# Kernel tuning notes

Measured on AMD Instinct MI355X. Metric: run time of the kernel, lower is better.

The kernel has to match this reference:

```python
import jax, jax.numpy as jnp
import numpy as np

GROUP_SIZE = 256


def dequantize(qweight, scales, zeros, dtype):
    # qweight: [out, in] uint8-valued ints; scales/zeros: [n_groups, 1]
    out_f, in_f = qweight.shape
    w = qweight.astype(dtype).reshape(-1, GROUP_SIZE)
    w = (w - zeros) * scales
    return w.reshape(out_f, in_f)


def setup_inputs() -> dict:
    key = jax.random.key(0)
    k1, k2, k3, k4, k5 = jax.random.split(key, 5)
    B, S, IN, OUT = 4, 2048, 4096, 4096
    n_groups = OUT * IN // GROUP_SIZE
    x = jax.random.normal(k1, (B, S, IN), dtype=jnp.float32)
    qweight = jax.random.randint(k2, (OUT, IN), 0, 256, dtype=jnp.int32)
    scales = jax.random.uniform(k3, (n_groups, 1), dtype=jnp.float32) * 0.01 + 1e-4
    zeros = jax.random.randint(k4, (n_groups, 1), 0, 256).astype(jnp.float32)
    bias = jax.random.normal(k5, (OUT,), dtype=jnp.float32) * 0.02
    return {"x": x, "qweight": qweight, "scales": scales, "zeros": zeros, "bias": bias}


def reference(x, qweight, scales, zeros, bias):
    # float_weight = (qw - zeros) * scales, grouped along flattened weight
    w = dequantize(qweight, scales, zeros, x.dtype)  # [out, in]
    # y = x @ W^T + b
    return jnp.einsum("bsi,oi->bso", x, w) + bias
```

## Files before the change

### kernel.cpp

```cpp
#include <hip/hip_runtime.h>


typedef __attribute__((ext_vector_type(8))) short bf16x8;
typedef __attribute__((ext_vector_type(8))) unsigned short ushort8;
typedef __attribute__((ext_vector_type(4))) float f32x4;

__device__ inline unsigned short f2bf(float f) {
  union { float f; unsigned int u; } v; v.f = f;
  unsigned int u = v.u;
  return (unsigned short)((u + 0x7fffu + ((u >> 16) & 1u)) >> 16);
}

__global__ void prep_kernel(const int* __restrict__ q,
                            const float* __restrict__ sc,
                            const float* __restrict__ zp,
                            ushort8* __restrict__ wb,
                            const float* __restrict__ x,
                            ushort8* __restrict__ xb,
                            int nw8, int nx8) {
  int t = blockIdx.x * blockDim.x + threadIdx.x;
  if (t < nw8) {
    const int4* q4 = (const int4*)q + (size_t)t * 2;
    int4 a = q4[0];
    int4 b = q4[1];
    int g = t >> 5;
    float s = sc[g], z = zp[g];
    ushort8 o;
    o[0] = f2bf(((float)a.x - z) * s);
    o[1] = f2bf(((float)a.y - z) * s);
    o[2] = f2bf(((float)a.z - z) * s);
    o[3] = f2bf(((float)a.w - z) * s);
    o[4] = f2bf(((float)b.x - z) * s);
    o[5] = f2bf(((float)b.y - z) * s);
    o[6] = f2bf(((float)b.z - z) * s);
    o[7] = f2bf(((float)b.w - z) * s);
    wb[t] = o;
  } else {
    int u = t - nw8;
    if (u >= nx8) return;
    const float4* x4 = (const float4*)x + (size_t)u * 2;
    float4 a = x4[0];
    float4 b = x4[1];
    ushort8 o;
    o[0] = f2bf(a.x); o[1] = f2bf(a.y); o[2] = f2bf(a.z); o[3] = f2bf(a.w);
    o[4] = f2bf(b.x); o[5] = f2bf(b.y); o[6] = f2bf(b.z); o[7] = f2bf(b.w);
    xb[u] = o;
  }
}

#define BM 256
#define BN 256
#define BK 64

#define BAR() asm volatile("s_barrier" ::: "memory")
#define MFMA16(d, x, y) d = __builtin_amdgcn_mfma_f32_16x16x32_bf16(x, y, d, 0, 0, 0)

__device__ inline void gload_lds16(const void* g, void* l) {
  __builtin_amdgcn_global_load_lds(
      (const __attribute__((address_space(1))) unsigned int*)g,
      (__attribute__((address_space(3))) unsigned int*)l, 16, 0, 0);
}

__device__ inline void stage_half(const unsigned short* __restrict__ gsrc,
                                  char* lds_region, int K, int wave, int lane) {
  const int l3  = lane >> 3;
  const int swz = ((lane & 7) ^ l3) * 8;
#pragma unroll
  for (int inst = 0; inst < 2; ++inst) {
    const int row = inst * 64 + wave * 8 + l3;
    gload_lds16(gsrc + (size_t)row * K + swz,
                lds_region + (size_t)(inst * 512 + wave * 64) * 16);
  }
}

__global__ __launch_bounds__(512, 2)
void gemm256_kernel(const unsigned short* __restrict__ A,
                    const unsigned short* __restrict__ B,
                    const float* __restrict__ bias,
                    float* __restrict__ C,
                    int M, int N, int K) {
  extern __shared__ char lds[];
  const int t    = threadIdx.x;
  const int lane = t & 63;
  const int wave = t >> 6;
  const int wm   = wave >> 2;
  const int wn   = wave & 3;
  const int lr   = lane & 15;
  const int hi   = lane >> 4;
  const int l7   = lane & 7;

  const int nwg = gridDim.x;
  const int cpx = nwg >> 3;
  const int bid = blockIdx.x;
  const int swzb = (bid & 7) * cpx + (bid >> 3);
  const int ntn = N / BN;
  const int bm = swzb / ntn, bn = swzb % ntn;
  const int row0 = bm * BM, col0 = bn * BN;

  const int NT = K / BK;

  const int soff0 = ((hi) ^ l7) * 16;
  const int soff1 = ((4 + hi) ^ l7) * 16;

  const unsigned short* Asrc = A + (size_t)row0 * K;
  const unsigned short* Bsrc = B + (size_t)col0 * K;

#define STAGE_A0(buf, kt) stage_half(Asrc + (size_t)(kt) * BK,           (buf),         K, wave, lane)
#define STAGE_A1(buf, kt) stage_half(Asrc + (size_t)128 * K + (kt) * BK, (buf) + 16384, K, wave, lane)
#define STAGE_B0(buf, kt) stage_half(Bsrc + (size_t)(kt) * BK,           (buf) + 32768, K, wave, lane)
#define STAGE_B1(buf, kt) stage_half(Bsrc + (size_t)128 * K + (kt) * BK, (buf) + 49152, K, wave, lane)

  f32x4 acc[8][4] = {};
  bf16x8 a[4][2];
  bf16x8 b[4][2];

#define READ_A(mh, bufp) {                                                    \
    const char* Ab_ = (const char*)(bufp) + wm * 16384 + (mh) * 8192;         \
    _Pragma("unroll")                                                         \
    for (int mm = 0; mm < 4; ++mm) {                                          \
      const int r_ = (mm * 16 + lr) * 128;                                    \
      a[mm][0] = *(const bf16x8*)(Ab_ + r_ + soff0);                          \
      a[mm][1] = *(const bf16x8*)(Ab_ + r_ + soff1);                          \
    } }
#define READ_B(nh, bufp) {                                                    \
    const char* Bb_ = (const char*)(bufp) + 32768 + wn * 8192;                \
    _Pragma("unroll")                                                         \
    for (int nn = 0; nn < 2; ++nn) {                                          \
      const int r_ = (((nh) * 2 + nn) * 16 + lr) * 128;                       \
      b[(nh) * 2 + nn][0] = *(const bf16x8*)(Bb_ + r_ + soff0);               \
      b[(nh) * 2 + nn][1] = *(const bf16x8*)(Bb_ + r_ + soff1);               \
    } }
#define MFMA_QUAD(mh, nh)                                                     \
    __builtin_amdgcn_s_setprio(1);                                            \
    _Pragma("unroll")                                                         \
    for (int mm = 0; mm < 4; ++mm)                                            \
      _Pragma("unroll")                                                       \
      for (int nn = 0; nn < 2; ++nn) {                                        \
        MFMA16(acc[(mh) * 4 + mm][(nh) * 2 + nn], a[mm][0], b[(nh) * 2 + nn][0]); \
        MFMA16(acc[(mh) * 4 + mm][(nh) * 2 + nn], a[mm][1], b[(nh) * 2 + nn][1]); \
      }                                                                       \
    __builtin_amdgcn_s_setprio(0);

#define KT_BODY(buf, nbuf, kt, GUARDED)                                       \
  {                                                                           \
                      \
    BAR();                                                                    \
    MFMA_QUAD(0, 0);                                                          \
    if (!(GUARDED) || (kt) + 1 < NT) STAGE_A1(nbuf, (kt) + 1);                \
    READ_B(1, buf);                                                           \
                     \
    BAR();                                                                    \
    MFMA_QUAD(0, 1);                                                          \
    if (!(GUARDED) || (kt) + 2 < NT) STAGE_B0(buf, (kt) + 2);                 \
    READ_A(1, buf);                                                           \
                          \
    BAR();                                                                    \
    MFMA_QUAD(1, 0);                                                          \
    if (!(GUARDED) || (kt) + 2 < NT) {                                        \
      STAGE_B1(buf, (kt) + 2);                                                \
      asm volatile("s_waitcnt vmcnt(4)" ::: "memory");                        \
    } else {                                                                  \
      asm volatile("s_waitcnt vmcnt(0)" ::: "memory");                        \
    }                                                                         \
       \
    BAR();                                                                    \
    MFMA_QUAD(1, 1);                                                          \
    if (!(GUARDED) || (kt) + 2 < NT) STAGE_A0(buf, (kt) + 2);                 \
    if (!(GUARDED) || (kt) + 1 < NT) {                                        \
      READ_A(0, nbuf);                                                        \
      READ_B(0, nbuf);                                                        \
    }                                                                         \
  }

  char* buf0 = lds;
  char* buf1 = lds + 65536;
  STAGE_A0(buf0, 0); STAGE_A1(buf0, 0); STAGE_B0(buf0, 0); STAGE_B1(buf0, 0);
  STAGE_A0(buf1, 1); STAGE_B0(buf1, 1); STAGE_B1(buf1, 1);
  asm volatile("s_waitcnt vmcnt(6)" ::: "memory");
  BAR();
  READ_A(0, buf0);
  READ_B(0, buf0);

  int kt = 0;
  for (; kt + 3 < NT; kt += 2) {
    KT_BODY(buf0, buf1, kt, 0);
    KT_BODY(buf1, buf0, kt + 1, 0);
  }
  for (; kt < NT; ++kt) {
    char* buf  = lds + ((kt & 1) << 16);
    char* nbuf = lds + (((kt & 1) ^ 1) << 16);
    KT_BODY(buf, nbuf, kt, 1);
  }

#pragma unroll
  for (int n = 0; n < 4; ++n) {
    const int col = col0 + wn * 64 + n * 16 + lr;
    const float bv = bias[col];
#pragma unroll
    for (int m = 0; m < 8; ++m) {
      const int rbase = row0 + wm * 128 + m * 16 + hi * 4;
#pragma unroll
      for (int j = 0; j < 4; ++j)
        C[(size_t)(rbase + j) * N + col] = acc[m][n][j] + bv;
    }
  }
#undef STAGE_A0
#undef STAGE_A1
#undef STAGE_B0
#undef STAGE_B1
#undef READ_A
#undef READ_B
#undef MFMA_QUAD
#undef KT_BODY
}

extern "C" void kernel_launch(void* const* d_in, const int* in_sizes, int n_in,
                              void* d_out, int out_size, void* d_ws, size_t ws_size,
                              hipStream_t stream) {
  const float* x      = (const float*)d_in[0];
  const int*   qw     = (const int*)d_in[1];
  const float* scales = (const float*)d_in[2];
  const float* zeros  = (const float*)d_in[3];
  const float* bias   = (const float*)d_in[4];
  float* out = (float*)d_out;

  const int OUT = in_sizes[4];
  const int IN  = in_sizes[1] / OUT;
  const int M   = in_sizes[0] / IN;

  unsigned short* wb = (unsigned short*)d_ws;
  unsigned short* xb = wb + (size_t)OUT * IN;

  {
    int nw8 = OUT * IN / 8;
    int nx8 = (int)((size_t)M * IN / 8);
    int total = nw8 + nx8;
    prep_kernel<<<(total + 255) / 256, 256, 0, stream>>>(
        qw, scales, zeros, (ushort8*)wb, x, (ushort8*)xb, nw8, nx8);
  }
  {
    hipFuncSetAttribute((const void*)gemm256_kernel,
                        hipFuncAttributeMaxDynamicSharedMemorySize, 131072);
    dim3 grid((M / BM) * (OUT / BN));
    gemm256_kernel<<<grid, 512, 131072, stream>>>(xb, wb, bias, out, M, OUT, IN);
  }
}
```

Baseline: 268.7 us.

## Halve GEMM K-tile to 32 with new LDS swizzle and grid-stride prep kernel

The GEMM K tile drops from 64 to 32, which halves the double-buffered LDS footprint from 128KB to 64KB. The staging layout, swizzle pattern, fragment reads and vmcnt waits are reworked to match. The smaller footprint is meant to let two workgroups fit per CU, as the launch bounds request. The prep kernel becomes a grid-stride loop over a fixed 2048-block grid instead of one thread per 8 elements. The cost is twice as many K iterations, with more barriers and staging overhead per unit of MFMA work, and less latency hiding per stage.

```diff
diff --git a/kernel.cpp b/kernel.cpp
--- a/kernel.cpp
+++ b/kernel.cpp
@@ -18,39 +18,40 @@
                             const float* __restrict__ x,
                             ushort8* __restrict__ xb,
                             int nw8, int nx8) {
-  int t = blockIdx.x * blockDim.x + threadIdx.x;
-  if (t < nw8) {
-    const int4* q4 = (const int4*)q + (size_t)t * 2;
-    int4 a = q4[0];
-    int4 b = q4[1];
-    int g = t >> 5;
-    float s = sc[g], z = zp[g];
-    ushort8 o;
-    o[0] = f2bf(((float)a.x - z) * s);
-    o[1] = f2bf(((float)a.y - z) * s);
-    o[2] = f2bf(((float)a.z - z) * s);
-    o[3] = f2bf(((float)a.w - z) * s);
-    o[4] = f2bf(((float)b.x - z) * s);
-    o[5] = f2bf(((float)b.y - z) * s);
-    o[6] = f2bf(((float)b.z - z) * s);
-    o[7] = f2bf(((float)b.w - z) * s);
-    wb[t] = o;
-  } else {
-    int u = t - nw8;
-    if (u >= nx8) return;
-    const float4* x4 = (const float4*)x + (size_t)u * 2;
-    float4 a = x4[0];
-    float4 b = x4[1];
-    ushort8 o;
-    o[0] = f2bf(a.x); o[1] = f2bf(a.y); o[2] = f2bf(a.z); o[3] = f2bf(a.w);
-    o[4] = f2bf(b.x); o[5] = f2bf(b.y); o[6] = f2bf(b.z); o[7] = f2bf(b.w);
-    xb[u] = o;
+  const int stride = gridDim.x * blockDim.x;
+  for (int t = blockIdx.x * blockDim.x + threadIdx.x; t < nw8 + nx8; t += stride) {
+    if (t < nw8) {
+      const int4* q4 = (const int4*)q + (size_t)t * 2;
+      int4 a = q4[0];
+      int4 b = q4[1];
+      int g = t >> 5;
+      float s = sc[g], z = zp[g];
+      ushort8 o;
+      o[0] = f2bf(((float)a.x - z) * s);
+      o[1] = f2bf(((float)a.y - z) * s);
+      o[2] = f2bf(((float)a.z - z) * s);
+      o[3] = f2bf(((float)a.w - z) * s);
+      o[4] = f2bf(((float)b.x - z) * s);
+      o[5] = f2bf(((float)b.y - z) * s);
+      o[6] = f2bf(((float)b.z - z) * s);
+      o[7] = f2bf(((float)b.w - z) * s);
+      wb[t] = o;
+    } else {
+      int u = t - nw8;
+      const float4* x4 = (const float4*)x + (size_t)u * 2;
+      float4 a = x4[0];
+      float4 b = x4[1];
+      ushort8 o;
+      o[0] = f2bf(a.x); o[1] = f2bf(a.y); o[2] = f2bf(a.z); o[3] = f2bf(a.w);
+      o[4] = f2bf(b.x); o[5] = f2bf(b.y); o[6] = f2bf(b.z); o[7] = f2bf(b.w);
+      xb[u] = o;
+    }
   }
 }
 
 #define BM 256
 #define BN 256
-#define BK 64
+#define BK 32
 
 #define BAR() asm volatile("s_barrier" ::: "memory")
 #define MFMA16(d, x, y) d = __builtin_amdgcn_mfma_f32_16x16x32_bf16(x, y, d, 0, 0, 0)
@@ -61,16 +62,12 @@
       (__attribute__((address_space(3))) unsigned int*)l, 16, 0, 0);
 }
 
-__device__ inline void stage_half(const unsigned short* __restrict__ gsrc,
-                                  char* lds_region, int K, int wave, int lane) {
-  const int l3  = lane >> 3;
-  const int swz = ((lane & 7) ^ l3) * 8;
-#pragma unroll
-  for (int inst = 0; inst < 2; ++inst) {
-    const int row = inst * 64 + wave * 8 + l3;
-    gload_lds16(gsrc + (size_t)row * K + swz,
-                lds_region + (size_t)(inst * 512 + wave * 64) * 16);
-  }
+__device__ inline void stage_unit32(const unsigned short* __restrict__ gsrc,
+                                    char* lds_region, int K, int wave, int lane) {
+  const int row  = wave * 16 + (lane >> 2);
+  const int slot = (lane & 3) ^ ((row >> 1) & 3);
+  gload_lds16(gsrc + (size_t)row * K + slot * 8,
+              lds_region + (size_t)wave * 1024);
 }
 
 __global__ __launch_bounds__(512, 2)
@@ -87,7 +84,6 @@
   const int wn   = wave & 3;
   const int lr   = lane & 15;
   const int hi   = lane >> 4;
-  const int l7   = lane & 7;
 
   const int nwg = gridDim.x;
   const int cpx = nwg >> 3;
@@ -99,46 +95,39 @@
 
   const int NT = K / BK;
 
-  const int soff0 = ((hi) ^ l7) * 16;
-  const int soff1 = ((4 + hi) ^ l7) * 16;
+  const int soff = (hi ^ ((lr >> 1) & 3)) * 16;
 
   const unsigned short* Asrc = A + (size_t)row0 * K;
   const unsigned short* Bsrc = B + (size_t)col0 * K;
 
-#define STAGE_A0(buf, kt) stage_half(Asrc + (size_t)(kt) * BK,           (buf),         K, wave, lane)
-#define STAGE_A1(buf, kt) stage_half(Asrc + (size_t)128 * K + (kt) * BK, (buf) + 16384, K, wave, lane)
-#define STAGE_B0(buf, kt) stage_half(Bsrc + (size_t)(kt) * BK,           (buf) + 32768, K, wave, lane)
-#define STAGE_B1(buf, kt) stage_half(Bsrc + (size_t)128 * K + (kt) * BK, (buf) + 49152, K, wave, lane)
+#define STAGE_A0(buf, kt) stage_unit32(Asrc + (size_t)(kt) * BK,           (buf),         K, wave, lane)
+#define STAGE_A1(buf, kt) stage_unit32(Asrc + (size_t)128 * K + (kt) * BK, (buf) + 8192,  K, wave, lane)
+#define STAGE_B0(buf, kt) stage_unit32(Bsrc + (size_t)(kt) * BK,           (buf) + 16384, K, wave, lane)
+#define STAGE_B1(buf, kt) stage_unit32(Bsrc + (size_t)128 * K + (kt) * BK, (buf) + 24576, K, wave, lane)
 
   f32x4 acc[8][4] = {};
-  bf16x8 a[4][2];
-  bf16x8 b[4][2];
+  bf16x8 a[4];
+  bf16x8 b[4];
 
 #define READ_A(mh, bufp) {                                                    \
-    const char* Ab_ = (const char*)(bufp) + wm * 16384 + (mh) * 8192;         \
+    const char* Ab_ = (const char*)(bufp) + wm * 8192 + (mh) * 4096;          \
     _Pragma("unroll")                                                         \
-    for (int mm = 0; mm < 4; ++mm) {                                          \
-      const int r_ = (mm * 16 + lr) * 128;                                    \
-      a[mm][0] = *(const bf16x8*)(Ab_ + r_ + soff0);                          \
-      a[mm][1] = *(const bf16x8*)(Ab_ + r_ + soff1);                          \
-    } }
+    for (int mm = 0; mm < 4; ++mm)                                            \
+      a[mm] = *(const bf16x8*)(Ab_ + (mm * 16 + lr) * 64 + soff);             \
+  }
 #define READ_B(nh, bufp) {                                                    \
-    const char* Bb_ = (const char*)(bufp) + 32768 + wn * 8192;                \
+    const char* Bb_ = (const char*)(bufp) + 16384 + (wn >> 1) * 8192 + (wn & 1) * 4096; \
     _Pragma("unroll")                                                         \
-    for (int nn = 0; nn < 2; ++nn) {                                          \
-      const int r_ = (((nh) * 2 + nn) * 16 + lr) * 128;                       \
-      b[(nh) * 2 + nn][0] = *(const bf16x8*)(Bb_ + r_ + soff0);               \
-      b[(nh) * 2 + nn][1] = *(const bf16x8*)(Bb_ + r_ + soff1);               \
-    } }
+    for (int nn = 0; nn < 2; ++nn)                                            \
+      b[(nh) * 2 + nn] = *(const bf16x8*)(Bb_ + (((nh) * 2 + nn) * 16 + lr) * 64 + soff); \
+  }
 #define MFMA_QUAD(mh, nh)                                                     \
     __builtin_amdgcn_s_setprio(1);                                            \
     _Pragma("unroll")                                                         \
     for (int mm = 0; mm < 4; ++mm)                                            \
       _Pragma("unroll")                                                       \
-      for (int nn = 0; nn < 2; ++nn) {                                        \
-        MFMA16(acc[(mh) * 4 + mm][(nh) * 2 + nn], a[mm][0], b[(nh) * 2 + nn][0]); \
-        MFMA16(acc[(mh) * 4 + mm][(nh) * 2 + nn], a[mm][1], b[(nh) * 2 + nn][1]); \
-      }                                                                       \
+      for (int nn = 0; nn < 2; ++nn)                                          \
+        MFMA16(acc[(mh) * 4 + mm][(nh) * 2 + nn], a[mm], b[(nh) * 2 + nn]);   \
     __builtin_amdgcn_s_setprio(0);
 
 #define KT_BODY(buf, nbuf, kt, GUARDED)                                       \
@@ -158,7 +147,7 @@
     MFMA_QUAD(1, 0);                                                          \
     if (!(GUARDED) || (kt) + 2 < NT) {                                        \
       STAGE_B1(buf, (kt) + 2);                                                \
-      asm volatile("s_waitcnt vmcnt(4)" ::: "memory");                        \
+      asm volatile("s_waitcnt vmcnt(2)" ::: "memory");                        \
     } else {                                                                  \
       asm volatile("s_waitcnt vmcnt(0)" ::: "memory");                        \
     }                                                                         \
@@ -173,10 +162,10 @@
   }
 
   char* buf0 = lds;
-  char* buf1 = lds + 65536;
+  char* buf1 = lds + 32768;
   STAGE_A0(buf0, 0); STAGE_A1(buf0, 0); STAGE_B0(buf0, 0); STAGE_B1(buf0, 0);
   STAGE_A0(buf1, 1); STAGE_B0(buf1, 1); STAGE_B1(buf1, 1);
-  asm volatile("s_waitcnt vmcnt(6)" ::: "memory");
+  asm volatile("s_waitcnt vmcnt(3)" ::: "memory");
   BAR();
   READ_A(0, buf0);
   READ_B(0, buf0);
@@ -187,8 +176,8 @@
     KT_BODY(buf1, buf0, kt + 1, 0);
   }
   for (; kt < NT; ++kt) {
-    char* buf  = lds + ((kt & 1) << 16);
-    char* nbuf = lds + (((kt & 1) ^ 1) << 16);
+    char* buf  = lds + ((kt & 1) << 15);
+    char* nbuf = lds + (((kt & 1) ^ 1) << 15);
     KT_BODY(buf, nbuf, kt, 1);
   }
 
@@ -234,14 +223,13 @@
   {
     int nw8 = OUT * IN / 8;
     int nx8 = (int)((size_t)M * IN / 8);
-    int total = nw8 + nx8;
-    prep_kernel<<<(total + 255) / 256, 256, 0, stream>>>(
+    prep_kernel<<<2048, 256, 0, stream>>>(
         qw, scales, zeros, (ushort8*)wb, x, (ushort8*)xb, nw8, nx8);
   }
   {
     hipFuncSetAttribute((const void*)gemm256_kernel,
-                        hipFuncAttributeMaxDynamicSharedMemorySize, 131072);
+                        hipFuncAttributeMaxDynamicSharedMemorySize, 65536);
     dim3 grid((M / BM) * (OUT / BN));
-    gemm256_kernel<<<grid, 512, 131072, stream>>>(xb, wb, bias, out, M, OUT, IN);
-  }
-}
+    gemm256_kernel<<<grid, 512, 65536, stream>>>(xb, wb, bias, out, M, OUT, IN);
+  }
+}
```

Result: slower. 284.0 us (+5.7%).
